# Performance work log

Measured on AMD Instinct MI355X. Metric: run time of the kernel, lower is better.

Reference implementation:

```python
import jax, jax.numpy as jnp
import numpy as np

HEAD_NUM = 6

def setup_inputs() -> dict:
    key = jax.random.key(0)
    k1, k2, k3 = jax.random.split(key, 3)
    B, N, P, C = 4, 64, 256, 384
    x = jax.random.normal(k1, (B, N, P, C), dtype=jnp.float32)
    # torch Linear init scale ~ 1/sqrt(fan_in); keep magnitudes sane
    w_qkv = jax.random.normal(k2, (C, 3 * C), dtype=jnp.float32) * (1.0 / np.sqrt(C))
    w_proj = jax.random.normal(k3, (C, C), dtype=jnp.float32) * (1.0 / np.sqrt(C))
    b_proj = jnp.zeros((C,), dtype=jnp.float32)
    return {"x": x, "w_qkv": w_qkv, "w_proj": w_proj, "b_proj": b_proj}

def reference(x, w_qkv, w_proj, b_proj):
    B, N, P, C = x.shape
    H = HEAD_NUM
    D = C // H
    scale = jnp.asarray(D, dtype=x.dtype)  # NOTE: head_dim ** 1, faithful to source
    qkv = (x @ w_qkv).reshape(B, N, P, 3, H, D)
    q = qkv[:, :, :, 0]  # (B, N, P, H, D)
    k = qkv[:, :, :, 1]
    v = qkv[:, :, :, 2]
    attn = jnp.einsum('bnphd,bnqhd->bnhpq', q, k) * scale  # (B,N,H,P,P)
    attn = jax.nn.softmax(attn, axis=-1)
    out = jnp.einsum('bnhpq,bnqhd->bnphd', attn, v).reshape(B, N, P, C)
    return out @ w_proj + b_proj
```

## Files before the change

kernel.cpp:

```cpp
#include <hip/hip_runtime.h>

typedef __bf16 bf16_t;
typedef __bf16 bf16x8 __attribute__((ext_vector_type(8)));
typedef float f32x4 __attribute__((ext_vector_type(4)));
typedef unsigned short u16;
typedef unsigned short u16x4 __attribute__((ext_vector_type(4)));
typedef unsigned int u32;

#define B_ 4
#define N_ 64
#define P_ 256
#define C_ 384
#define H_ 6
#define D_ 64
#define M_TOTAL 65536
#define NQKV 1152
#define KSTEPS 12
#define NBLK (H_*B_*N_)
#define WKS_U16 10240
#define WKS_BYTES 20480
#define FUSED_LDS 131072
#define PB_STRIDE 40
#define SB() __builtin_amdgcn_sched_barrier(0)

#define GLOAD_LDS16(g, l) __builtin_amdgcn_global_load_lds( \
    (const __attribute__((address_space(1))) void*)(g), \
    (__attribute__((address_space(3))) void*)(l), 16, 0, 0)
#define GLOAD_LDS4(g, l) __builtin_amdgcn_global_load_lds( \
    (const __attribute__((address_space(1))) void*)(g), \
    (__attribute__((address_space(3))) void*)(l), 4, 0, 0)

__device__ __forceinline__ u16 f2b(float f){ return __builtin_bit_cast(u16, (bf16_t)f); }
__device__ __forceinline__ f32x4 mfma(bf16x8 a, bf16x8 b, f32x4 c){
    return __builtin_amdgcn_mfma_f32_16x16x32_bf16(a, b, c, 0, 0, 0);
}

__global__ __launch_bounds__(256) void prep_w(
    const float* __restrict__ wqkv, const float* __restrict__ wproj,
    u16* __restrict__ Wpk, u16* __restrict__ wPt)
{
    int i = blockIdx.x * 256 + threadIdx.x;
    const int NSLOT = H_ * KSTEPS * 12 * 64;
    if (i < NSLOT) {
        int lane = i & 63;
        int frag = i >> 6;
        int nf = frag % 12;
        int ks = (frag / 12) % KSTEPS;
        int h  = frag / (12 * KSTEPS);
        int part = nf >> 2;
        int nh   = (nf & 3) * 16 + (lane & 15);
        int col  = part * C_ + h * 64 + nh;
        int k0   = ks * 32 + (lane >> 4) * 8;
        size_t base = (size_t)(h * KSTEPS + ks) * WKS_U16;
        #pragma unroll
        for (int e = 0; e < 8; ++e) {
            float w = wqkv[(size_t)(k0 + e) * NQKV + col];
            bf16_t hi = (bf16_t)w;
            Wpk[base + nf * 512 + lane * 8 + e] = __builtin_bit_cast(u16, hi);
            if (nf < 8)
                Wpk[base + 6144 + nf * 512 + lane * 8 + e] = f2b(w - (float)hi);
        }
    }
    int j = i - NSLOT;
    if (j >= 0 && j < C_ * C_) {
        int k = j / C_, n = j % C_;
        wPt[(size_t)n * C_ + k] = f2b(wproj[j]);
    }
}

__global__ __launch_bounds__(1024, 4) void fused_attn(
    const float* __restrict__ x, const u16* __restrict__ Wpk,
    u16* __restrict__ attn)
{
    extern __shared__ u16 sm[];
    u16* Kh = sm;
    u16* Kl = sm + 16384;
    u16* Vt = sm + 32768;

    const int tid  = threadIdx.x;
    const int lane = tid & 63, wid = tid >> 6;
    const int g = lane >> 4, r16 = lane & 15;

    const int p = blockIdx.x;
    const int logical = (p & 7) * (NBLK / 8) + (p >> 3);
    const int h  = logical % H_;
    const int bn = logical / H_;
    const size_t row0 = (size_t)bn * P_;
    const int m0w = wid * 16;

    f32x4 acc[12];
    #pragma unroll
    for (int nf = 0; nf < 12; ++nf) acc[nf] = f32x4{0.f,0.f,0.f,0.f};

    const float* xr0 = x + (row0 + m0w + r16) * C_;
    const char* wbase = (const char*)Wpk + (size_t)h * (KSTEPS * WKS_BYTES);

#define STAGE(ks_, b_) do { \
    const char* _gp = wbase + (size_t)(ks_) * WKS_BYTES; \
    char* _lp = (char*)(sm + (b_) * WKS_U16); \
    GLOAD_LDS16(_gp + tid * 16, _lp + tid * 16); \
    GLOAD_LDS4(_gp + 16384 + tid * 4, _lp + 16384 + tid * 4); \
} while (0)

    f32x4 xr[2][2];
#define XLOAD(ks_, par_) do { \
    const float* _xp = xr0 + (ks_) * 32 + 8 * g; \
    xr[par_][0] = *(const f32x4*)_xp; xr[par_][1] = *(const f32x4*)(_xp + 4); \
} while (0)

    bf16x8 ah, al;
#define SPLIT_A(par_) do { \
    _Pragma("unroll") \
    for (int e = 0; e < 4; ++e) { \
        bf16_t h0 = (bf16_t)xr[par_][0][e], h1 = (bf16_t)xr[par_][1][e]; \
        ah[e]   = h0; al[e]   = (bf16_t)(xr[par_][0][e] - (float)h0); \
        ah[4+e] = h1; al[4+e] = (bf16_t)(xr[par_][1][e] - (float)h1); \
    } } while (0)

    STAGE(0, 0);
    XLOAD(0, 0);
    STAGE(1, 1);
    SB();
    asm volatile("s_waitcnt vmcnt(2)" ::: "memory");
    __builtin_amdgcn_s_barrier();
    SB();

    #pragma unroll
    for (int ks = 0; ks < KSTEPS; ++ks) {
        const int par = ks & 1, nxt = par ^ 1;
        if (ks + 2 < KSTEPS) STAGE(ks + 2, (ks + 2) % 3);
        if (ks + 1 < KSTEPS) XLOAD(ks + 1, nxt);
        SPLIT_A(par);

        const u16* stg = sm + (ks % 3) * WKS_U16;
        #pragma unroll
        for (int nf = 0; nf < 8; ++nf) {
            bf16x8 bh = *(const bf16x8*)&stg[nf * 512 + lane * 8];
            bf16x8 bl = *(const bf16x8*)&stg[6144 + nf * 512 + lane * 8];
            acc[nf] = mfma(ah, bh, acc[nf]);
            acc[nf] = mfma(ah, bl, acc[nf]);
            acc[nf] = mfma(al, bh, acc[nf]);
        }
        #pragma unroll
        for (int nf = 8; nf < 12; ++nf) {
            bf16x8 bh = *(const bf16x8*)&stg[nf * 512 + lane * 8];
            acc[nf] = mfma(ah, bh, acc[nf]);
        }

        if (ks < KSTEPS - 1) {
            SB();
            if (ks + 2 < KSTEPS) asm volatile("s_waitcnt vmcnt(4)" ::: "memory");
            else                 asm volatile("s_waitcnt vmcnt(2)" ::: "memory");
            __builtin_amdgcn_s_barrier();
            SB();
        } else {
            __syncthreads();
        }
    }

    #pragma unroll
    for (int f = 0; f < 4; ++f) {
        const int d = f * 16 + r16;
        const int q0 = m0w + 4 * g;
        u16x4 vv;
        #pragma unroll
        for (int rr = 0; rr < 4; ++rr) vv[rr] = f2b(acc[8 + f][rr]);
        *(u16x4*)&Vt[d * 256 + (((q0 >> 3) ^ (d & 7)) << 3) + (q0 & 7)] = vv;
        #pragma unroll
        for (int rr = 0; rr < 4; ++rr) {
            int q = q0 + rr;
            int ek = q * 64 + (((d >> 3) ^ (q & 7)) << 3) + (d & 7);
            float kv = acc[4 + f][rr];
            bf16_t khi = (bf16_t)kv;
            Kh[ek] = __builtin_bit_cast(u16, khi);
            Kl[ek] = f2b(kv - (float)khi);
        }
    }

    u16* myQb = sm + 49152 + wid * 1024;
    bf16x8 aqh[2], aql[2];
    #pragma unroll
    for (int f = 0; f < 4; ++f)
    #pragma unroll
    for (int rr = 0; rr < 4; ++rr) {
        int r = 4 * g + rr;
        int c = f * 16 + r16;
        myQb[r * 64 + (((c >> 3) ^ (r & 7)) << 3) + (c & 7)] = f2b(acc[f][rr]);
    }
    #pragma unroll
    for (int k2 = 0; k2 < 2; ++k2)
        aqh[k2] = *(const bf16x8*)&myQb[r16 * 64 + (((k2 * 4 + g) ^ (r16 & 7)) << 3)];
    SB();
    #pragma unroll
    for (int f = 0; f < 4; ++f)
    #pragma unroll
    for (int rr = 0; rr < 4; ++rr) {
        int r = 4 * g + rr;
        int c = f * 16 + r16;
        float v = acc[f][rr];
        bf16_t hi = (bf16_t)v;
        myQb[r * 64 + (((c >> 3) ^ (r & 7)) << 3) + (c & 7)] = f2b(v - (float)hi);
    }
    #pragma unroll
    for (int k2 = 0; k2 < 2; ++k2)
        aql[k2] = *(const bf16x8*)&myQb[r16 * 64 + (((k2 * 4 + g) ^ (r16 & 7)) << 3)];

    __syncthreads();

    f32x4 S[16];
    #pragma unroll
    for (int nf = 0; nf < 16; ++nf) S[nf] = f32x4{0.f,0.f,0.f,0.f};

    const int kb0 = r16 * 64 + (((0 * 4 + g) ^ (r16 & 7)) << 3);
    const int kb1 = r16 * 64 + (((1 * 4 + g) ^ (r16 & 7)) << 3);

    bf16x8 khv[2][2], klv[2][2];
    {
        khv[0][0] = *(const bf16x8*)&Kh[kb0];
        klv[0][0] = *(const bf16x8*)&Kl[kb0];
        khv[0][1] = *(const bf16x8*)&Kh[kb1];
        klv[0][1] = *(const bf16x8*)&Kl[kb1];
    }
    #pragma unroll
    for (int nf = 0; nf < 16; ++nf) {
        const int par = nf & 1, nxt = par ^ 1;
        if (nf < 15) {
            const int o = (nf + 1) * 1024;
            khv[nxt][0] = *(const bf16x8*)&Kh[o + kb0];
            klv[nxt][0] = *(const bf16x8*)&Kl[o + kb0];
            khv[nxt][1] = *(const bf16x8*)&Kh[o + kb1];
            klv[nxt][1] = *(const bf16x8*)&Kl[o + kb1];
        }
        SB();
        __builtin_amdgcn_s_setprio(1);
        #pragma unroll
        for (int k2 = 0; k2 < 2; ++k2) {
            S[nf] = mfma(khv[par][k2], aqh[k2], S[nf]);
            S[nf] = mfma(klv[par][k2], aqh[k2], S[nf]);
            S[nf] = mfma(khv[par][k2], aql[k2], S[nf]);
        }
        __builtin_amdgcn_s_setprio(0);
        SB();
    }

    float inv_;
    {
        float m = -1e30f;
        #pragma unroll
        for (int nf = 0; nf < 16; ++nf)
            #pragma unroll
            for (int rr = 0; rr < 4; ++rr) m = fmaxf(m, S[nf][rr]);
        m = fmaxf(m, __shfl_xor(m, 16, 64));
        m = fmaxf(m, __shfl_xor(m, 32, 64));
        float s = 0.f;
        #pragma unroll
        for (int nf = 0; nf < 16; ++nf)
            #pragma unroll
            for (int rr = 0; rr < 4; ++rr) {
                float pv = __expf((S[nf][rr] - m) * 64.0f);
                S[nf][rr] = pv;
                s += pv;
            }
        s += __shfl_xor(s, 16, 64);
        s += __shfl_xor(s, 32, 64);
        inv_ = 1.0f / s;
    }

    f32x4 O[4];
    #pragma unroll
    for (int f = 0; f < 4; ++f) O[f] = f32x4{0.f,0.f,0.f,0.f};

    u16* pt = sm + 49152 + wid * 1024;
    const int vc = r16 & 7;
    #pragma unroll
    for (int t = 0; t < 8; ++t) {
        bf16x8 bv[4];
        const int vo = (((4 * t + g) ^ vc) << 3) + r16 * 256;
        #pragma unroll
        for (int f = 0; f < 4; ++f)
            bv[f] = *(const bf16x8*)&Vt[f * 4096 + vo];
        #pragma unroll
        for (int nu = 0; nu < 2; ++nu) {
            int nf = 2 * t + nu;
            u16x4 pk;
            #pragma unroll
            for (int rr = 0; rr < 4; ++rr) pk[rr] = f2b(S[nf][rr] * inv_);
            *(u16x4*)&pt[r16 * PB_STRIDE + nu * 16 + 4 * g] = pk;
        }
        bf16x8 ap = *(const bf16x8*)&pt[r16 * PB_STRIDE + 8 * g];
        __builtin_amdgcn_s_setprio(1);
        #pragma unroll
        for (int f = 0; f < 4; ++f) O[f] = mfma(ap, bv[f], O[f]);
        __builtin_amdgcn_s_setprio(0);
    }

    #pragma unroll
    for (int f = 0; f < 4; ++f)
    #pragma unroll
    for (int rr = 0; rr < 4; ++rr)
        attn[(row0 + m0w + 4 * g + rr) * C_ + h * 64 + f * 16 + r16] = f2b(O[f][rr]);
}

__global__ __launch_bounds__(256, 2) void proj_kernel(
    const u16* __restrict__ attn, const u16* __restrict__ wPt,
    const float* __restrict__ bias, float* __restrict__ out)
{
    __shared__ alignas(16) u16 As[128*32];
    __shared__ alignas(16) u16 Bs[128*32];

    const int tid = threadIdx.x;
    const int lane = tid & 63, wid = tid >> 6;
    const int wr = wid >> 1, wc = wid & 1;
    const int g = lane >> 4, r16 = lane & 15;
    const int m0 = blockIdx.x * 128;
    const int n0 = blockIdx.y * 128;

    f32x4 acc[4][4];
    for (int i = 0; i < 4; i++) for (int j = 0; j < 4; j++) acc[i][j] = f32x4{0.f,0.f,0.f,0.f};

    for (int kt = 0; kt < C_; kt += 32) {
        for (int r = 0; r < 4; ++r) {
            int i = tid + 256*r;
            int mm = i >> 3;
            int kk = (i & 7) << 2;
            u16x4 v = *(const u16x4*)&attn[(size_t)(m0+mm)*C_ + kt + kk];
            int e = mm*32 + (((kk>>3) ^ ((mm>>1)&3))<<3) + (kk&7);
            *(u16x4*)&As[e] = v;
        }
        for (int r = 0; r < 4; ++r) {
            int i = tid + 256*r;
            int nn = i >> 3;
            int kk = (i & 7) << 2;
            u16x4 v = *(const u16x4*)&wPt[(size_t)(n0+nn)*C_ + kt + kk];
            int e = nn*32 + (((kk>>3) ^ ((nn>>1)&3))<<3) + (kk&7);
            *(u16x4*)&Bs[e] = v;
        }
        __syncthreads();

        bf16x8 a[4], b[4];
        for (int i = 0; i < 4; i++) {
            int row = wr*64 + i*16 + r16;
            a[i] = *(const bf16x8*)&As[row*32 + ((g ^ ((row>>1)&3))<<3)];
        }
        for (int j = 0; j < 4; j++) {
            int n = wc*64 + j*16 + r16;
            b[j] = *(const bf16x8*)&Bs[n*32 + ((g ^ ((n>>1)&3))<<3)];
        }
        for (int i = 0; i < 4; i++) for (int j = 0; j < 4; j++)
            acc[i][j] = mfma(a[i], b[j], acc[i][j]);
        __syncthreads();
    }

    for (int i = 0; i < 4; i++) for (int j = 0; j < 4; j++) for (int rr = 0; rr < 4; rr++) {
        size_t row = m0 + wr*64 + i*16 + g*4 + rr;
        int col = n0 + wc*64 + j*16 + r16;
        out[row*C_ + col] = acc[i][j][rr] + bias[col];
    }
}

extern "C" void kernel_launch(void* const* d_in, const int* in_sizes, int n_in,
                              void* d_out, int out_size, void* d_ws, size_t ws_size,
                              hipStream_t stream)
{
    const float* x      = (const float*)d_in[0];
    const float* w_qkv  = (const float*)d_in[1];
    const float* w_proj = (const float*)d_in[2];
    const float* b_proj = (const float*)d_in[3];
    float* out = (float*)d_out;

    u16* ws = (u16*)d_ws;
    u16* attnb = ws;
    size_t off = (size_t)M_TOTAL * C_;
    u16* Wpk = ws + off; off += (size_t)H_ * KSTEPS * WKS_U16;
    u16* wPt = ws + off; off += (size_t)C_ * C_;

    hipFuncSetAttribute((const void*)fused_attn,
                        hipFuncAttributeMaxDynamicSharedMemorySize, FUSED_LDS);

    int prep_n = H_ * KSTEPS * 12 * 64 + C_ * C_;
    prep_w<<<dim3((prep_n + 255) / 256), 256, 0, stream>>>(w_qkv, w_proj, Wpk, wPt);
    fused_attn<<<dim3(NBLK), 1024, FUSED_LDS, stream>>>(x, Wpk, attnb);
    proj_kernel<<<dim3(M_TOTAL / 128, C_ / 128), 256, 0, stream>>>(attnb, wPt, b_proj, out);
}
```

Before: 236.7 us.

## Restructure projection GEMM with full-N tiles, pre-packed weights and async LDS pipelining

The projection kernel now gives each 512-thread block a 128-row strip across all 384 output columns. Weights are pre-packed into MFMA fragment layout, and tiles are loaded with double-buffered global_load_lds so the next k-step prefetches while the current one computes. This reads the attention activations once instead of three times and removes register staging and swizzle arithmetic. The weight prep is split into two kernels that transpose through LDS for coalesced reads. The cost is higher register pressure from 24 accumulators per wave and more LDS per block.

Result: no change. 241.2 us (+1.9%).

```diff
diff --git a/kernel.cpp b/kernel.cpp
--- a/kernel.cpp
+++ b/kernel.cpp
@@ -21,6 +21,7 @@
 #define WKS_BYTES 20480
 #define FUSED_LDS 131072
 #define PB_STRIDE 40
+#define PROJ_LDS 65536
 #define SB() __builtin_amdgcn_sched_barrier(0)
 
 #define GLOAD_LDS16(g, l) __builtin_amdgcn_global_load_lds( \
@@ -35,36 +36,67 @@
     return __builtin_amdgcn_mfma_f32_16x16x32_bf16(a, b, c, 0, 0, 0);
 }
 
-__global__ __launch_bounds__(256) void prep_w(
-    const float* __restrict__ wqkv, const float* __restrict__ wproj,
-    u16* __restrict__ Wpk, u16* __restrict__ wPt)
+__global__ __launch_bounds__(256) void prep_attn(
+    const float* __restrict__ wqkv, u16* __restrict__ Wpk)
 {
-    int i = blockIdx.x * 256 + threadIdx.x;
-    const int NSLOT = H_ * KSTEPS * 12 * 64;
-    if (i < NSLOT) {
-        int lane = i & 63;
-        int frag = i >> 6;
-        int nf = frag % 12;
-        int ks = (frag / 12) % KSTEPS;
-        int h  = frag / (12 * KSTEPS);
+    __shared__ float tile[32][192];
+    const int h  = blockIdx.x / KSTEPS;
+    const int ks = blockIdx.x % KSTEPS;
+    const int tid = threadIdx.x;
+
+    #pragma unroll
+    for (int it = 0; it < 24; ++it) {
+        int idx = tid + 256 * it;
+        int row = idx / 192, cc = idx % 192;
+        int part = cc / 64, c = cc % 64;
+        tile[row][cc] = wqkv[(size_t)(ks * 32 + row) * NQKV + part * C_ + h * 64 + c];
+    }
+    __syncthreads();
+
+    const size_t base = (size_t)(h * KSTEPS + ks) * WKS_U16;
+    #pragma unroll
+    for (int it = 0; it < 3; ++it) {
+        int slot = tid + 256 * it;
+        int nf = slot >> 6, lane = slot & 63;
+        int r16 = lane & 15, g = lane >> 4;
         int part = nf >> 2;
-        int nh   = (nf & 3) * 16 + (lane & 15);
-        int col  = part * C_ + h * 64 + nh;
-        int k0   = ks * 32 + (lane >> 4) * 8;
-        size_t base = (size_t)(h * KSTEPS + ks) * WKS_U16;
+        int cc = part * 64 + (nf & 3) * 16 + r16;
         #pragma unroll
         for (int e = 0; e < 8; ++e) {
-            float w = wqkv[(size_t)(k0 + e) * NQKV + col];
+            float w = tile[g * 8 + e][cc];
             bf16_t hi = (bf16_t)w;
             Wpk[base + nf * 512 + lane * 8 + e] = __builtin_bit_cast(u16, hi);
             if (nf < 8)
                 Wpk[base + 6144 + nf * 512 + lane * 8 + e] = f2b(w - (float)hi);
         }
     }
-    int j = i - NSLOT;
-    if (j >= 0 && j < C_ * C_) {
-        int k = j / C_, n = j % C_;
-        wPt[(size_t)n * C_ + k] = f2b(wproj[j]);
+}
+
+__global__ __launch_bounds__(256) void prep_proj(
+    const float* __restrict__ wproj, u16* __restrict__ wPj)
+{
+    __shared__ float tile[32][384];
+    const int ks = blockIdx.x;
+    const int tid = threadIdx.x;
+
+    #pragma unroll
+    for (int it = 0; it < 48; ++it) {
+        int idx = tid + 256 * it;
+        int row = idx / 384, n = idx % 384;
+        tile[row][n] = wproj[(size_t)(ks * 32 + row) * C_ + n];
+    }
+    __syncthreads();
+
+    const size_t base = (size_t)ks * 12288;
+    #pragma unroll
+    for (int it = 0; it < 6; ++it) {
+        int slot = tid + 256 * it;
+        int nf = slot >> 6, lane = slot & 63;
+        int r16 = lane & 15, g = lane >> 4;
+        int n = nf * 16 + r16;
+        #pragma unroll
+        for (int e = 0; e < 8; ++e)
+            wPj[base + nf * 512 + lane * 8 + e] = f2b(tile[g * 8 + e][n]);
     }
 }
 
@@ -301,60 +333,66 @@
         attn[(row0 + m0w + 4 * g + rr) * C_ + h * 64 + f * 16 + r16] = f2b(O[f][rr]);
 }
 
-__global__ __launch_bounds__(256, 2) void proj_kernel(
-    const u16* __restrict__ attn, const u16* __restrict__ wPt,
+__global__ __launch_bounds__(512, 2) void proj_kernel(
+    const u16* __restrict__ attn, const u16* __restrict__ wPj,
     const float* __restrict__ bias, float* __restrict__ out)
 {
-    __shared__ alignas(16) u16 As[128*32];
-    __shared__ alignas(16) u16 Bs[128*32];
-
+    extern __shared__ u16 psm[];
     const int tid = threadIdx.x;
     const int lane = tid & 63, wid = tid >> 6;
-    const int wr = wid >> 1, wc = wid & 1;
+    const int rw = wid >> 1, cw = wid & 1;
     const int g = lane >> 4, r16 = lane & 15;
-    const int m0 = blockIdx.x * 128;
-    const int n0 = blockIdx.y * 128;
-
-    f32x4 acc[4][4];
-    for (int i = 0; i < 4; i++) for (int j = 0; j < 4; j++) acc[i][j] = f32x4{0.f,0.f,0.f,0.f};
-
-    for (int kt = 0; kt < C_; kt += 32) {
-        for (int r = 0; r < 4; ++r) {
-            int i = tid + 256*r;
-            int mm = i >> 3;
-            int kk = (i & 7) << 2;
-            u16x4 v = *(const u16x4*)&attn[(size_t)(m0+mm)*C_ + kt + kk];
-            int e = mm*32 + (((kk>>3) ^ ((mm>>1)&3))<<3) + (kk&7);
-            *(u16x4*)&As[e] = v;
-        }
-        for (int r = 0; r < 4; ++r) {
-            int i = tid + 256*r;
-            int nn = i >> 3;
-            int kk = (i & 7) << 2;
-            u16x4 v = *(const u16x4*)&wPt[(size_t)(n0+nn)*C_ + kt + kk];
-            int e = nn*32 + (((kk>>3) ^ ((nn>>1)&3))<<3) + (kk&7);
-            *(u16x4*)&Bs[e] = v;
+    const size_t m0 = (size_t)blockIdx.x * 128;
+
+#define PSTAGE(ks_, b_) do { \
+    const u16* _as = attn + (m0 + (tid >> 2)) * C_ + (ks_) * 32 + (tid & 3) * 8; \
+    GLOAD_LDS16(_as, (char*)(psm + (b_) * 4096) + tid * 16); \
+    const u16* _bs = wPj + (size_t)(ks_) * 12288; \
+    char* _bl = (char*)(psm + 8192 + (b_) * 12288); \
+    GLOAD_LDS16(_bs + tid * 8,            _bl + tid * 16); \
+    GLOAD_LDS16(_bs + 4096 + tid * 8,     _bl + 8192 + tid * 16); \
+    GLOAD_LDS16(_bs + 8192 + tid * 8,     _bl + 16384 + tid * 16); \
+} while (0)
+
+    f32x4 acc[2][12];
+    #pragma unroll
+    for (int mf = 0; mf < 2; ++mf)
+        #pragma unroll
+        for (int nf = 0; nf < 12; ++nf) acc[mf][nf] = f32x4{0.f,0.f,0.f,0.f};
+
+    PSTAGE(0, 0);
+    __syncthreads();
+
+    for (int ks = 0; ks < KSTEPS; ++ks) {
+        const int cur = ks & 1, nxt = cur ^ 1;
+        if (ks + 1 < KSTEPS) PSTAGE(ks + 1, nxt);
+
+        const u16* Ab = psm + cur * 4096;
+        const u16* Bb = psm + 8192 + cur * 12288;
+        bf16x8 a[2];
+        #pragma unroll
+        for (int mf = 0; mf < 2; ++mf)
+            a[mf] = *(const bf16x8*)&Ab[(rw * 32 + mf * 16 + r16) * 32 + 8 * g];
+        #pragma unroll
+        for (int nf = 0; nf < 12; ++nf) {
+            bf16x8 b = *(const bf16x8*)&Bb[(cw * 12 + nf) * 512 + lane * 8];
+            acc[0][nf] = mfma(a[0], b, acc[0][nf]);
+            acc[1][nf] = mfma(a[1], b, acc[1][nf]);
         }
         __syncthreads();
-
-        bf16x8 a[4], b[4];
-        for (int i = 0; i < 4; i++) {
-            int row = wr*64 + i*16 + r16;
-            a[i] = *(const bf16x8*)&As[row*32 + ((g ^ ((row>>1)&3))<<3)];
-        }
-        for (int j = 0; j < 4; j++) {
-            int n = wc*64 + j*16 + r16;
-            b[j] = *(const bf16x8*)&Bs[n*32 + ((g ^ ((n>>1)&3))<<3)];
-        }
-        for (int i = 0; i < 4; i++) for (int j = 0; j < 4; j++)
-            acc[i][j] = mfma(a[i], b[j], acc[i][j]);
-        __syncthreads();
-    }
-
-    for (int i = 0; i < 4; i++) for (int j = 0; j < 4; j++) for (int rr = 0; rr < 4; rr++) {
-        size_t row = m0 + wr*64 + i*16 + g*4 + rr;
-        int col = n0 + wc*64 + j*16 + r16;
-        out[row*C_ + col] = acc[i][j][rr] + bias[col];
+    }
+
+    #pragma unroll
+    for (int mf = 0; mf < 2; ++mf)
+    #pragma unroll
+    for (int nf = 0; nf < 12; ++nf) {
+        int col = cw * 192 + nf * 16 + r16;
+        float bb = bias[col];
+        #pragma unroll
+        for (int rr = 0; rr < 4; ++rr) {
+            size_t row = m0 + rw * 32 + mf * 16 + 4 * g + rr;
+            out[row * C_ + col] = acc[mf][nf][rr] + bb;
+        }
     }
 }
 
@@ -372,13 +410,15 @@
     u16* attnb = ws;
     size_t off = (size_t)M_TOTAL * C_;
     u16* Wpk = ws + off; off += (size_t)H_ * KSTEPS * WKS_U16;
-    u16* wPt = ws + off; off += (size_t)C_ * C_;
+    u16* wPj = ws + off; off += (size_t)KSTEPS * 12288;
 
     hipFuncSetAttribute((const void*)fused_attn,
                         hipFuncAttributeMaxDynamicSharedMemorySize, FUSED_LDS);
-
-    int prep_n = H_ * KSTEPS * 12 * 64 + C_ * C_;
-    prep_w<<<dim3((prep_n + 255) / 256), 256, 0, stream>>>(w_qkv, w_proj, Wpk, wPt);
+    hipFuncSetAttribute((const void*)proj_kernel,
+                        hipFuncAttributeMaxDynamicSharedMemorySize, PROJ_LDS);
+
+    prep_attn<<<dim3(H_ * KSTEPS), 256, 0, stream>>>(w_qkv, Wpk);
+    prep_proj<<<dim3(KSTEPS), 256, 0, stream>>>(w_proj, wPj);
     fused_attn<<<dim3(NBLK), 1024, FUSED_LDS, stream>>>(x, Wpk, attnb);
-    proj_kernel<<<dim3(M_TOTAL / 128, C_ / 128), 256, 0, stream>>>(attnb, wPt, b_proj, out);
-}
+    proj_kernel<<<dim3(M_TOTAL / 128), 512, PROJ_LDS, stream>>>(attnb, wPj, b_proj, out);
+}
```
